# Kernel optimization log

Measured on AMD Instinct MI355X. Metric: run time of the kernel, lower is better.

Reference implementation:

```python
import jax, jax.numpy as jnp
import numpy as np

WIDTH = 256
HEAD = 16
SCALE = 2
G = WIDTH // HEAD          # 16 groups
NH = G * SCALE             # 32 kernelized heads
EPS = 1e-5
N_NODES = 20000
B_GRAPHS = 1024


def setup_inputs() -> dict:
    key = jax.random.key(0)
    ks = jax.random.split(key, 10)
    x = jax.random.normal(ks[0], (N_NODES, WIDTH), jnp.float32)
    x_res = jax.random.normal(ks[1], (B_GRAPHS, NH, HEAD, HEAD), jnp.float32)
    batch = jnp.sort(jax.random.randint(ks[2], (N_NODES,), 0, B_GRAPHS)).astype(jnp.int64)
    w_pre = jax.random.normal(ks[3], (WIDTH, WIDTH), jnp.float32) * 0.02
    b_pre = jnp.zeros((WIDTH,), jnp.float32)
    # grouped 1x1 convs: [groups, width_scale, head_out, head_in]
    wq = jax.random.normal(ks[4], (G, SCALE, HEAD, HEAD), jnp.float32) * 0.02
    wk = jax.random.normal(ks[5], (G, SCALE, HEAD, HEAD), jnp.float32) * 0.02
    wv = jax.random.normal(ks[6], (G, SCALE, HEAD, HEAD), jnp.float32) * 0.02
    w_post = jax.random.normal(ks[7], (WIDTH, WIDTH * SCALE), jnp.float32) * 0.02
    b_post = jnp.zeros((WIDTH,), jnp.float32)
    log_scale = jnp.full((WIDTH,), np.log(0.01), jnp.float32)
    return {"x": x, "x_res": x_res, "batch": batch, "batch_size": B_GRAPHS,
            "w_pre": w_pre, "b_pre": b_pre, "wq": wq, "wk": wk, "wv": wv,
            "w_post": w_post, "b_post": b_post, "log_scale": log_scale}


def reference(x, x_res, batch, batch_size, w_pre, b_pre, wq, wk, wv, w_post, b_post, log_scale):
    n = x.shape[0]
    # pre: 1x1 conv (= linear) + GroupNorm(affine=False); L=1 so normalize over
    # each group's width_head channels.
    y = x @ w_pre.T + b_pre                       # [N, width]
    yg = y.reshape(n, G, HEAD)                    # [N, G, Hd]
    mu = yg.mean(-1, keepdims=True)
    var = yg.var(-1, keepdims=True)               # biased, as in GroupNorm
    yn = (yg - mu) / jnp.sqrt(var + EPS)          # [N, G, Hd]

    inv_sqrt_h = 1.0 / np.sqrt(HEAD)
    # grouped convs -> kernelized q,k (exp) and v
    xq = jnp.exp(jnp.einsum('ngi,gsoi->ngso', yn, wq) * inv_sqrt_h).reshape(n, NH, HEAD)
    xk = jnp.exp(jnp.einsum('ngi,gsoi->ngso', yn, wk) * inv_sqrt_h).reshape(n, NH, HEAD)
    xv = jnp.einsum('ngi,gsoi->ngso', yn, wv).reshape(n, NH, HEAD)

    # outer product k (x) v then scatter-sum over graphs  [B, NH, Hd, Hd]
    kv = jnp.einsum('bnh,bnv->bnhv', xk, xv)
    kv_sum = jax.ops.segment_sum(kv, batch, num_segments=batch_size) + x_res
    x_res_out = kv_sum

    # per-graph key sum, gathered back to nodes
    k_sum = jax.ops.segment_sum(xk, batch, num_segments=batch_size)[batch]  # [N, NH, Hd]
    denom = jnp.einsum('bnh,bnh->bn', xq, k_sum)                            # [N, NH]
    qn = xq / denom[:, :, None]

    out = jnp.einsum('bnh,bnhv->bnv', qn, kv_sum[batch]).reshape(n, WIDTH * SCALE)
    out = jnp.exp(log_scale) * (out @ w_post.T + b_post)                    # [N, width]
    return (out, x_res_out)
```

## Files before the change

### kernel.cpp

```cpp
#include <hip/hip_runtime.h>
#include <stdint.h>

typedef unsigned int u32;
typedef unsigned short u16;
typedef __attribute__((ext_vector_type(8))) short v8s;
typedef __attribute__((ext_vector_type(4))) float v4f;

#define GN_EPS 1e-5f

__device__ __forceinline__ float bflo(u32 u){ return __uint_as_float(u << 16); }
__device__ __forceinline__ float bfhi(u32 u){ return __uint_as_float(u & 0xffff0000u); }
__device__ __forceinline__ float bf1(u16 u){ return __uint_as_float((u32)u << 16); }
__device__ __forceinline__ u16 f2bf(float f){
  u32 x = __float_as_uint(f);
  u32 r = (x + 0x7fffu + ((x >> 16) & 1u)) >> 16;
  return (u16)r;
}
__device__ __forceinline__ u32 pack2(float a, float b){
  return (u32)f2bf(a) | ((u32)f2bf(b) << 16);
}
__device__ __forceinline__ void unpack8(const uint4 u, float* f){
  f[0]=bflo(u.x); f[1]=bfhi(u.x); f[2]=bflo(u.y); f[3]=bfhi(u.y);
  f[4]=bflo(u.z); f[5]=bfhi(u.z); f[6]=bflo(u.w); f[7]=bfhi(u.w);
}
__device__ __forceinline__ uint4 loadpack8(const float* __restrict__ p){
  float4 a = *(const float4*)p, b = *(const float4*)(p + 4);
  return make_uint4(pack2(a.x,a.y),pack2(a.z,a.w),pack2(b.x,b.y),pack2(b.z,b.w));
}

__device__ __forceinline__ int getb(const int* __restrict__ b, int is64, int i){
  return b[is64 ? 2*i : i];
}

__global__ __launch_bounds__(256) void k_detect(
    const int* __restrict__ batch, int n, int* __restrict__ flags)
{
  int i = blockIdx.x*256 + threadIdx.x;
  int bad = 0;
  if (i < n - 1 && batch[i] > batch[i + 1]) bad = 1;
  if (__builtin_amdgcn_ballot_w64(bad) != 0 && (threadIdx.x & 63) == 0)
    atomicOr(&flags[0], 1);
}

__global__ __launch_bounds__(256) void k_bounds(
    const int* __restrict__ batch, const int* __restrict__ flags,
    int N, int B, int* __restrict__ bounds)
{
  int i = blockIdx.x*256 + threadIdx.x;
  if (i >= N) return;
  const int is64 = flags[0];
  int b = getb(batch, is64, i);
  int prev = (i == 0) ? -1 : getb(batch, is64, i - 1);
  for (int g = prev + 1; g <= b; g++) bounds[g] = i;
  if (i == N - 1)
    for (int g = b + 1; g <= B; g++) bounds[g] = N;
}

__global__ __launch_bounds__(256) void k_pre(
    const float* __restrict__ x, const float* __restrict__ wpre,
    const float* __restrict__ bpre, u16* __restrict__ y, int N, int nbm)
{
  __shared__ __align__(16) u16 As[128*40];
  __shared__ __align__(16) u16 Bs[64*40];
  const int t = threadIdx.x;
  const int bm = blockIdx.x % nbm;
  const int bn = blockIdx.x / nbm;
  const int m_base = bm*128, n_base = bn*64;
  const int w = t >> 6, lane = t & 63;
  const int wr = (w >> 1)*64, wc = (w & 1)*32;
  const int fr = lane & 15, fk = lane >> 4;
  const int arow = t >> 1, acol = (t & 1)*16;
  const int brow = t >> 2, bcol = (t & 3)*8;

  v4f acc[4][2];
#pragma unroll
  for (int i = 0; i < 4; i++)
#pragma unroll
    for (int j = 0; j < 2; j++) acc[i][j] = (v4f){0.f,0.f,0.f,0.f};

  for (int k0 = 0; k0 < 256; k0 += 32) {
    __syncthreads();
    {
      int gm = m_base + arow;
      uint4 a0 = make_uint4(0u,0u,0u,0u), a1 = make_uint4(0u,0u,0u,0u);
      if (gm < N) {
        a0 = loadpack8(x + (size_t)gm*256 + k0 + acol);
        a1 = loadpack8(x + (size_t)gm*256 + k0 + acol + 8);
      }
      *(uint4*)&As[arow*40 + acol]     = a0;
      *(uint4*)&As[arow*40 + acol + 8] = a1;
      uint4 bv = loadpack8(wpre + (size_t)(n_base + brow)*256 + k0 + bcol);
      *(uint4*)&Bs[brow*40 + bcol] = bv;
    }
    __syncthreads();
    v8s b0 = *(const v8s*)&Bs[(wc      + fr)*40 + fk*8];
    v8s b1 = *(const v8s*)&Bs[(wc + 16 + fr)*40 + fk*8];
#pragma unroll
    for (int mi = 0; mi < 4; mi++) {
      v8s a = *(const v8s*)&As[(wr + mi*16 + fr)*40 + fk*8];
      acc[mi][0] = __builtin_amdgcn_mfma_f32_16x16x32_bf16(a,b0,acc[mi][0],0,0,0);
      acc[mi][1] = __builtin_amdgcn_mfma_f32_16x16x32_bf16(a,b1,acc[mi][1],0,0,0);
    }
  }
#pragma unroll
  for (int nj = 0; nj < 2; nj++) {
    int col = n_base + wc + nj*16 + fr;
    float bpv = bpre[col];
#pragma unroll
    for (int mi = 0; mi < 4; mi++) {
#pragma unroll
      for (int r = 0; r < 4; r++) {
        int row = m_base + wr + mi*16 + fk*4 + r;
        if (row < N) y[(size_t)row*256 + col] = f2bf(acc[mi][nj][r] + bpv);
      }
    }
  }
}

__global__ __launch_bounds__(256) void k_gnqkv(
    const u16* __restrict__ y, const float* __restrict__ wq,
    const float* __restrict__ wk, const float* __restrict__ wv,
    u16* __restrict__ qo, u16* __restrict__ ko, u16* __restrict__ vo, int N)
{
  __shared__ __align__(16) float wL[3*512];
  const int t = threadIdx.x;
  const int g = blockIdx.x & 15;
  const int c = blockIdx.x >> 4;
  {
    const float* srcs[3] = {wq, wk, wv};
#pragma unroll
    for (int tz = 0; tz < 3; tz++) {
      wL[tz*512 + t]       = srcs[tz][g*512 + t];
      wL[tz*512 + t + 256] = srcs[tz][g*512 + t + 256];
    }
  }
  __syncthreads();
  const int node = c*256 + t;
  if (node >= N) return;

  const u16* yp = y + (size_t)node*256 + g*16;
  uint4 Y0 = *(const uint4*)yp;
  uint4 Y1 = *(const uint4*)(yp + 8);
  float a[16]; unpack8(Y0, a); unpack8(Y1, a + 8);
  float mu = 0.f;
#pragma unroll
  for (int i = 0; i < 16; i++) mu += a[i];
  mu *= 0.0625f;
  float s2 = 0.f;
#pragma unroll
  for (int i = 0; i < 16; i++) { float d = a[i]-mu; s2 = fmaf(d,d,s2); }
  float inv = rsqrtf(s2*0.0625f + GN_EPS);
  float yn[16];
#pragma unroll
  for (int i = 0; i < 16; i++) yn[i] = (a[i]-mu)*inv;

  u16* outs[3] = {qo, ko, vo};
#pragma unroll
  for (int tz = 0; tz < 3; tz++) {
#pragma unroll
    for (int s = 0; s < 2; s++) {
      u32 p[8];
#pragma unroll
      for (int o = 0; o < 16; o++) {
        const float* row = &wL[tz*512 + (s*16 + o)*16];
        float4 W0 = *(const float4*)row;
        float4 W1 = *(const float4*)(row + 4);
        float4 W2 = *(const float4*)(row + 8);
        float4 W3 = *(const float4*)(row + 12);
        float w[16] = {W0.x,W0.y,W0.z,W0.w,W1.x,W1.y,W1.z,W1.w,
                       W2.x,W2.y,W2.z,W2.w,W3.x,W3.y,W3.z,W3.w};
        float d = 0.f;
#pragma unroll
        for (int i = 0; i < 16; i++) d = fmaf(yn[i], w[i], d);
        if (tz < 2) d = __expf(d*0.25f);
        if (o & 1) p[o>>1] |= (u32)f2bf(d) << 16;
        else       p[o>>1]  = (u32)f2bf(d);
      }
      u16* dst = outs[tz] + (size_t)node*512 + g*32 + s*16;
      *(uint4*)dst       = make_uint4(p[0],p[1],p[2],p[3]);
      *(uint4*)(dst + 8) = make_uint4(p[4],p[5],p[6],p[7]);
    }
  }
}

__global__ __launch_bounds__(512) void k_segatt(
    const u16* __restrict__ xk, const u16* __restrict__ xv,
    const u16* __restrict__ xq, const float* __restrict__ xres,
    const int* __restrict__ bounds,
    float* __restrict__ out1, u16* __restrict__ att, int N)
{
  __shared__ __align__(16) u16 kvs[32*280];
  __shared__ float kss[32*17];
  const int b = blockIdx.x, t = threadIdx.x;
  const int lo = bounds[b], hi = bounds[b+1];
  const int nh = t >> 4, d = t & 15;

  float kv[16];
#pragma unroll
  for (int v = 0; v < 16; v++) kv[v] = 0.f;
  float ks = 0.f;

  const size_t koff = (size_t)nh*16 + d;
  const size_t voff = (size_t)nh*16;
  int node = lo;
  for (; node + 1 < hi; node += 2) {
    u16  ka  = xk[(size_t)node*512 + koff];
    uint4 Va0 = *(const uint4*)(xv + (size_t)node*512 + voff);
    uint4 Va1 = *(const uint4*)(xv + (size_t)node*512 + voff + 8);
    u16  kb  = xk[(size_t)(node+1)*512 + koff];
    uint4 Vb0 = *(const uint4*)(xv + (size_t)(node+1)*512 + voff);
    uint4 Vb1 = *(const uint4*)(xv + (size_t)(node+1)*512 + voff + 8);
    float k0 = bf1(ka), k1 = bf1(kb);
    float va[16], vb[16];
    unpack8(Va0, va); unpack8(Va1, va + 8);
    unpack8(Vb0, vb); unpack8(Vb1, vb + 8);
    ks += k0 + k1;
#pragma unroll
    for (int v = 0; v < 16; v++) {
      kv[v] = fmaf(k0, va[v], kv[v]);
      kv[v] = fmaf(k1, vb[v], kv[v]);
    }
  }
  if (node < hi) {
    u16  ka  = xk[(size_t)node*512 + koff];
    uint4 V0 = *(const uint4*)(xv + (size_t)node*512 + voff);
    uint4 V1 = *(const uint4*)(xv + (size_t)node*512 + voff + 8);
    float k0 = bf1(ka);
    float vf[16]; unpack8(V0, vf); unpack8(V1, vf + 8);
    ks += k0;
#pragma unroll
    for (int v = 0; v < 16; v++) kv[v] = fmaf(k0, vf[v], kv[v]);
  }

  kss[nh*17 + d] = ks;

  {
    size_t idx = ((size_t)(b*32 + nh)*16 + d)*16;
    const float* xp = xres + idx;
    float4 X0 = *(const float4*)xp;
    float4 X1 = *(const float4*)(xp + 4);
    float4 X2 = *(const float4*)(xp + 8);
    float4 X3 = *(const float4*)(xp + 12);
    float xf[16] = {X0.x,X0.y,X0.z,X0.w,X1.x,X1.y,X1.z,X1.w,
                    X2.x,X2.y,X2.z,X2.w,X3.x,X3.y,X3.z,X3.w};
    float o[16];
#pragma unroll
    for (int j = 0; j < 16; j++) o[j] = kv[j] + xf[j];
    float* op = out1 + idx;
    *(float4*)op        = make_float4(o[0],o[1],o[2],o[3]);
    *(float4*)(op + 4)  = make_float4(o[4],o[5],o[6],o[7]);
    *(float4*)(op + 8)  = make_float4(o[8],o[9],o[10],o[11]);
    *(float4*)(op + 12) = make_float4(o[12],o[13],o[14],o[15]);
    u16* lp = &kvs[nh*280 + d*16];
    *(uint4*)lp       = make_uint4(pack2(o[0],o[1]),  pack2(o[2],o[3]),
                                   pack2(o[4],o[5]),  pack2(o[6],o[7]));
    *(uint4*)(lp + 8) = make_uint4(pack2(o[8],o[9]),  pack2(o[10],o[11]),
                                   pack2(o[12],o[13]),pack2(o[14],o[15]));
  }
  __syncthreads();

  const int nh2 = t & 31, ns = t >> 5;
  for (int n0 = lo; n0 < hi; n0 += 16) {
    int nodei = n0 + ns;
    if (nodei >= hi) continue;
    const u16* qp = xq + (size_t)nodei*512 + nh2*16;
    uint4 Q0 = *(const uint4*)qp;
    uint4 Q1 = *(const uint4*)(qp + 8);
    float q[16]; unpack8(Q0, q); unpack8(Q1, q + 8);
    const float* ksp = &kss[nh2*17];
    float denom = 0.f;
#pragma unroll
    for (int i = 0; i < 16; i++) denom = fmaf(q[i], ksp[i], denom);
    float inv = 1.0f / fmaxf(denom, 1e-20f);
    float a[16];
#pragma unroll
    for (int v = 0; v < 16; v++) a[v] = 0.f;
    const u16* kvp = &kvs[nh2*280];
#pragma unroll
    for (int h = 0; h < 16; h++) {
      float qh = q[h] * inv;
      uint4 W0 = *(const uint4*)(kvp + h*16);
      uint4 W1 = *(const uint4*)(kvp + h*16 + 8);
      float w[16]; unpack8(W0, w); unpack8(W1, w + 8);
#pragma unroll
      for (int v = 0; v < 16; v++) a[v] = fmaf(qh, w[v], a[v]);
    }
    u32 p[8];
#pragma unroll
    for (int j = 0; j < 8; j++) p[j] = pack2(a[2*j], a[2*j+1]);
    u16* dst = att + (size_t)nodei*512 + nh2*16;
    *(uint4*)dst       = make_uint4(p[0],p[1],p[2],p[3]);
    *(uint4*)(dst + 8) = make_uint4(p[4],p[5],p[6],p[7]);
  }
}

__global__ __launch_bounds__(256) void k_post(
    const u16* __restrict__ att, const float* __restrict__ wpost,
    const float* __restrict__ bpost, const float* __restrict__ ls,
    float* __restrict__ out0, int N, int nbm)
{
  __shared__ __align__(16) u16 As[128*40];
  __shared__ __align__(16) u16 Bs[64*40];
  const int t = threadIdx.x;
  const int bm = blockIdx.x % nbm;
  const int bn = blockIdx.x / nbm;
  const int m_base = bm*128, n_base = bn*64;
  const int w = t >> 6, lane = t & 63;
  const int wr = (w >> 1)*64, wc = (w & 1)*32;
  const int fr = lane & 15, fk = lane >> 4;
  const int arow = t >> 1, acol = (t & 1)*16;
  const int brow = t >> 2, bcol = (t & 3)*8;

  v4f acc[4][2];
#pragma unroll
  for (int i = 0; i < 4; i++)
#pragma unroll
    for (int j = 0; j < 2; j++) acc[i][j] = (v4f){0.f,0.f,0.f,0.f};

  for (int k0 = 0; k0 < 512; k0 += 32) {
    __syncthreads();
    {
      int gm = m_base + arow;
      uint4 a0 = make_uint4(0u,0u,0u,0u), a1 = make_uint4(0u,0u,0u,0u);
      if (gm < N) {
        a0 = *(const uint4*)(att + (size_t)gm*512 + k0 + acol);
        a1 = *(const uint4*)(att + (size_t)gm*512 + k0 + acol + 8);
      }
      *(uint4*)&As[arow*40 + acol]     = a0;
      *(uint4*)&As[arow*40 + acol + 8] = a1;
      uint4 bv = loadpack8(wpost + (size_t)(n_base + brow)*512 + k0 + bcol);
      *(uint4*)&Bs[brow*40 + bcol] = bv;
    }
    __syncthreads();
    v8s b0 = *(const v8s*)&Bs[(wc      + fr)*40 + fk*8];
    v8s b1 = *(const v8s*)&Bs[(wc + 16 + fr)*40 + fk*8];
#pragma unroll
    for (int mi = 0; mi < 4; mi++) {
      v8s a = *(const v8s*)&As[(wr + mi*16 + fr)*40 + fk*8];
      acc[mi][0] = __builtin_amdgcn_mfma_f32_16x16x32_bf16(a,b0,acc[mi][0],0,0,0);
      acc[mi][1] = __builtin_amdgcn_mfma_f32_16x16x32_bf16(a,b1,acc[mi][1],0,0,0);
    }
  }
#pragma unroll
  for (int nj = 0; nj < 2; nj++) {
    int col = n_base + wc + nj*16 + fr;
    float bpv = bpost[col];
    float e   = __expf(ls[col]);
#pragma unroll
    for (int mi = 0; mi < 4; mi++) {
#pragma unroll
      for (int r = 0; r < 4; r++) {
        int row = m_base + wr + mi*16 + fk*4 + r;
        if (row < N) out0[(size_t)row*256 + col] = e*(acc[mi][nj][r] + bpv);
      }
    }
  }
}

extern "C" void kernel_launch(void* const* d_in, const int* in_sizes, int n_in,
                              void* d_out, int out_size, void* d_ws, size_t ws_size,
                              hipStream_t stream)
{
  const float* x     = (const float*)d_in[0];
  const float* xres  = (const float*)d_in[1];
  const int*   batch = (const int*)d_in[2];
  const float* wpre  = (const float*)d_in[4];
  const float* bpre  = (const float*)d_in[5];
  const float* wq    = (const float*)d_in[6];
  const float* wk    = (const float*)d_in[7];
  const float* wv    = (const float*)d_in[8];
  const float* wpost = (const float*)d_in[9];
  const float* bpost = (const float*)d_in[10];
  const float* ls    = (const float*)d_in[11];

  const int N = in_sizes[0] / 256;
  const int B = in_sizes[1] / 8192;
  const int nbm = (N + 127) / 128;
  const int nchunk = (N + 255) / 256;

  char* ws = (char*)d_ws;
  size_t off = 0;
  int*   flags  = (int*)(ws + off); off += 256;
  int*   bounds = (int*)(ws + off); off += ((size_t)B + 64) * 4;
  u16*   y      = (u16*)(ws + off);  off += (size_t)N * 512;
  u16*   att    = (u16*)(ws + off);  off += (size_t)N * 1024;
  u16*   q      = (u16*)(ws + off);  off += (size_t)N * 1024;
  u16*   kten   = (u16*)(ws + off);  off += (size_t)N * 1024;
  u16*   vten   = (u16*)(ws + off);  off += (size_t)N * 1024;

  float* out0 = (float*)d_out;
  float* out1 = out0 + (size_t)N * 256;

  hipMemsetAsync(flags, 0, 4, stream);
  k_detect<<<nchunk,         256, 0, stream>>>(batch, N, flags);
  k_bounds<<<nchunk,         256, 0, stream>>>(batch, flags, N, B, bounds);
  k_pre   <<<nbm * 4,        256, 0, stream>>>(x, wpre, bpre, y, N, nbm);
  k_gnqkv <<<nchunk * 16,    256, 0, stream>>>(y, wq, wk, wv, q, kten, vten, N);
  k_segatt<<<B,              512, 0, stream>>>(kten, vten, q, xres, bounds,
                                               out1, att, N);
  k_post  <<<nbm * 4,        256, 0, stream>>>(att, wpost, bpost, ls, out0, N, nbm);
}
```

Measured before the change: 130.8 us.

## Fuse pre-linear GEMM with GroupNorm and grouped QKV projection

Merges the pre-projection GEMM and the GroupNorm plus q/k/v grouped-conv kernel into one kernel. GroupNorm statistics are computed from the MFMA accumulators with 16-lane shuffle reductions, the normalized values go to shared memory, and each block then computes q/k/v for its 4 groups using weights staged in reused LDS. This removes the bf16 y intermediate round trip through global memory and one launch. In exchange it adds LDS pressure, a single-pass variance formula, and only 128 nodes x 4 groups of projection work per block.

```diff
diff --git a/kernel.cpp b/kernel.cpp
--- a/kernel.cpp
+++ b/kernel.cpp
@@ -26,6 +26,30 @@
 __device__ __forceinline__ uint4 loadpack8(const float* __restrict__ p){
   float4 a = *(const float4*)p, b = *(const float4*)(p + 4);
   return make_uint4(pack2(a.x,a.y),pack2(a.z,a.w),pack2(b.x,b.y),pack2(b.z,b.w));
+}
+__device__ __forceinline__ float dot16(const float* __restrict__ yn,
+                                       const float* __restrict__ row){
+  float4 W0 = *(const float4*)row;
+  float4 W1 = *(const float4*)(row + 4);
+  float4 W2 = *(const float4*)(row + 8);
+  float4 W3 = *(const float4*)(row + 12);
+  float d = 0.f;
+  d = fmaf(yn[0],W0.x,d); d = fmaf(yn[1],W0.y,d);
+  d = fmaf(yn[2],W0.z,d); d = fmaf(yn[3],W0.w,d);
+  d = fmaf(yn[4],W1.x,d); d = fmaf(yn[5],W1.y,d);
+  d = fmaf(yn[6],W1.z,d); d = fmaf(yn[7],W1.w,d);
+  d = fmaf(yn[8],W2.x,d); d = fmaf(yn[9],W2.y,d);
+  d = fmaf(yn[10],W2.z,d); d = fmaf(yn[11],W2.w,d);
+  d = fmaf(yn[12],W3.x,d); d = fmaf(yn[13],W3.y,d);
+  d = fmaf(yn[14],W3.z,d); d = fmaf(yn[15],W3.w,d);
+  return d;
+}
+__device__ __forceinline__ float rsum16(float v){
+  v += __shfl_xor(v, 1);
+  v += __shfl_xor(v, 2);
+  v += __shfl_xor(v, 4);
+  v += __shfl_xor(v, 8);
+  return v;
 }
 
 __device__ __forceinline__ int getb(const int* __restrict__ b, int is64, int i){
@@ -56,12 +80,20 @@
     for (int g = b + 1; g <= B; g++) bounds[g] = N;
 }
 
-__global__ __launch_bounds__(256) void k_pre(
+__global__ __launch_bounds__(256) void k_prefused(
     const float* __restrict__ x, const float* __restrict__ wpre,
-    const float* __restrict__ bpre, u16* __restrict__ y, int N, int nbm)
-{
-  __shared__ __align__(16) u16 As[128*40];
-  __shared__ __align__(16) u16 Bs[64*40];
+    const float* __restrict__ bpre,
+    const float* __restrict__ wq, const float* __restrict__ wk,
+    const float* __restrict__ wv,
+    u16* __restrict__ qo, u16* __restrict__ ko, u16* __restrict__ vo,
+    int N, int nbm)
+{
+  __shared__ __align__(16) char SMEM[25600];
+  __shared__ __align__(16) u16 ynL[128*72];
+  u16* As = (u16*)SMEM;
+  u16* Bs = (u16*)(SMEM + 128*40*2);
+  float* wL = (float*)SMEM;
+
   const int t = threadIdx.x;
   const int bm = blockIdx.x % nbm;
   const int bn = blockIdx.x / nbm;
@@ -102,83 +134,68 @@
       acc[mi][1] = __builtin_amdgcn_mfma_f32_16x16x32_bf16(a,b1,acc[mi][1],0,0,0);
     }
   }
+
 #pragma unroll
   for (int nj = 0; nj < 2; nj++) {
     int col = n_base + wc + nj*16 + fr;
     float bpv = bpre[col];
+    int gloc = (w & 1)*2 + nj;
 #pragma unroll
     for (int mi = 0; mi < 4; mi++) {
 #pragma unroll
       for (int r = 0; r < 4; r++) {
-        int row = m_base + wr + mi*16 + fk*4 + r;
-        if (row < N) y[(size_t)row*256 + col] = f2bf(acc[mi][nj][r] + bpv);
-      }
-    }
-  }
-}
-
-__global__ __launch_bounds__(256) void k_gnqkv(
-    const u16* __restrict__ y, const float* __restrict__ wq,
-    const float* __restrict__ wk, const float* __restrict__ wv,
-    u16* __restrict__ qo, u16* __restrict__ ko, u16* __restrict__ vo, int N)
-{
-  __shared__ __align__(16) float wL[3*512];
-  const int t = threadIdx.x;
-  const int g = blockIdx.x & 15;
-  const int c = blockIdx.x >> 4;
+        float yv = acc[mi][nj][r] + bpv;
+        float s1 = rsum16(yv);
+        float s2 = rsum16(yv*yv);
+        float mu = s1 * 0.0625f;
+        float var = fmaxf(s2*0.0625f - mu*mu, 0.f);
+        float ynv = (yv - mu) * rsqrtf(var + GN_EPS);
+        int row = wr + mi*16 + fk*4 + r;
+        ynL[row*72 + gloc*16 + fr] = f2bf(ynv);
+      }
+    }
+  }
+  __syncthreads();
+
   {
     const float* srcs[3] = {wq, wk, wv};
 #pragma unroll
     for (int tz = 0; tz < 3; tz++) {
-      wL[tz*512 + t]       = srcs[tz][g*512 + t];
-      wL[tz*512 + t + 256] = srcs[tz][g*512 + t + 256];
+      for (int i = t; i < 2048; i += 256) {
+        int gi = i >> 9, rem = i & 511;
+        wL[tz*2080 + gi*520 + rem] = srcs[tz][((size_t)(bn*4 + gi))*512 + rem];
+      }
     }
   }
   __syncthreads();
-  const int node = c*256 + t;
-  if (node >= N) return;
-
-  const u16* yp = y + (size_t)node*256 + g*16;
-  uint4 Y0 = *(const uint4*)yp;
-  uint4 Y1 = *(const uint4*)(yp + 8);
-  float a[16]; unpack8(Y0, a); unpack8(Y1, a + 8);
-  float mu = 0.f;
-#pragma unroll
-  for (int i = 0; i < 16; i++) mu += a[i];
-  mu *= 0.0625f;
-  float s2 = 0.f;
-#pragma unroll
-  for (int i = 0; i < 16; i++) { float d = a[i]-mu; s2 = fmaf(d,d,s2); }
-  float inv = rsqrtf(s2*0.0625f + GN_EPS);
-  float yn[16];
-#pragma unroll
-  for (int i = 0; i < 16; i++) yn[i] = (a[i]-mu)*inv;
 
   u16* outs[3] = {qo, ko, vo};
 #pragma unroll
-  for (int tz = 0; tz < 3; tz++) {
-#pragma unroll
-    for (int s = 0; s < 2; s++) {
-      u32 p[8];
-#pragma unroll
-      for (int o = 0; o < 16; o++) {
-        const float* row = &wL[tz*512 + (s*16 + o)*16];
-        float4 W0 = *(const float4*)row;
-        float4 W1 = *(const float4*)(row + 4);
-        float4 W2 = *(const float4*)(row + 8);
-        float4 W3 = *(const float4*)(row + 12);
-        float w[16] = {W0.x,W0.y,W0.z,W0.w,W1.x,W1.y,W1.z,W1.w,
-                       W2.x,W2.y,W2.z,W2.w,W3.x,W3.y,W3.z,W3.w};
-        float d = 0.f;
-#pragma unroll
-        for (int i = 0; i < 16; i++) d = fmaf(yn[i], w[i], d);
-        if (tz < 2) d = __expf(d*0.25f);
-        if (o & 1) p[o>>1] |= (u32)f2bf(d) << 16;
-        else       p[o>>1]  = (u32)f2bf(d);
-      }
-      u16* dst = outs[tz] + (size_t)node*512 + g*32 + s*16;
-      *(uint4*)dst       = make_uint4(p[0],p[1],p[2],p[3]);
-      *(uint4*)(dst + 8) = make_uint4(p[4],p[5],p[6],p[7]);
+  for (int p = 0; p < 2; p++) {
+    int idx = p*256 + t;
+    int nloc = idx >> 2, gl = idx & 3;
+    int node = m_base + nloc;
+    if (node >= N) continue;
+    uint4 Y0 = *(const uint4*)&ynL[nloc*72 + gl*16];
+    uint4 Y1 = *(const uint4*)&ynL[nloc*72 + gl*16 + 8];
+    float yn[16]; unpack8(Y0, yn); unpack8(Y1, yn + 8);
+    int g = bn*4 + gl;
+#pragma unroll
+    for (int tz = 0; tz < 3; tz++) {
+#pragma unroll
+      for (int s = 0; s < 2; s++) {
+        u32 pk[8];
+#pragma unroll
+        for (int o = 0; o < 16; o++) {
+          float d = dot16(yn, &wL[tz*2080 + gl*520 + (s*16 + o)*16]);
+          if (tz < 2) d = __expf(d*0.25f);
+          if (o & 1) pk[o>>1] |= (u32)f2bf(d) << 16;
+          else       pk[o>>1]  = (u32)f2bf(d);
+        }
+        u16* dst = outs[tz] + (size_t)node*512 + g*32 + s*16;
+        *(uint4*)dst       = make_uint4(pk[0],pk[1],pk[2],pk[3]);
+        *(uint4*)(dst + 8) = make_uint4(pk[4],pk[5],pk[6],pk[7]);
+      }
     }
   }
 }
@@ -281,9 +298,9 @@
       float qh = q[h] * inv;
       uint4 W0 = *(const uint4*)(kvp + h*16);
       uint4 W1 = *(const uint4*)(kvp + h*16 + 8);
-      float w[16]; unpack8(W0, w); unpack8(W1, w + 8);
-#pragma unroll
-      for (int v = 0; v < 16; v++) a[v] = fmaf(qh, w[v], a[v]);
+      float wv2[16]; unpack8(W0, wv2); unpack8(W1, wv2 + 8);
+#pragma unroll
+      for (int v = 0; v < 16; v++) a[v] = fmaf(qh, wv2[v], a[v]);
     }
     u32 p[8];
 #pragma unroll
@@ -382,7 +399,6 @@
   size_t off = 0;
   int*   flags  = (int*)(ws + off); off += 256;
   int*   bounds = (int*)(ws + off); off += ((size_t)B + 64) * 4;
-  u16*   y      = (u16*)(ws + off);  off += (size_t)N * 512;
   u16*   att    = (u16*)(ws + off);  off += (size_t)N * 1024;
   u16*   q      = (u16*)(ws + off);  off += (size_t)N * 1024;
   u16*   kten   = (u16*)(ws + off);  off += (size_t)N * 1024;
@@ -392,11 +408,11 @@
   float* out1 = out0 + (size_t)N * 256;
 
   hipMemsetAsync(flags, 0, 4, stream);
-  k_detect<<<nchunk,         256, 0, stream>>>(batch, N, flags);
-  k_bounds<<<nchunk,         256, 0, stream>>>(batch, flags, N, B, bounds);
-  k_pre   <<<nbm * 4,        256, 0, stream>>>(x, wpre, bpre, y, N, nbm);
-  k_gnqkv <<<nchunk * 16,    256, 0, stream>>>(y, wq, wk, wv, q, kten, vten, N);
-  k_segatt<<<B,              512, 0, stream>>>(kten, vten, q, xres, bounds,
-                                               out1, att, N);
-  k_post  <<<nbm * 4,        256, 0, stream>>>(att, wpost, bpost, ls, out0, N, nbm);
-}
+  k_detect  <<<nchunk,        256, 0, stream>>>(batch, N, flags);
+  k_bounds  <<<nchunk,        256, 0, stream>>>(batch, flags, N, B, bounds);
+  k_prefused<<<nbm * 4,       256, 0, stream>>>(x, wpre, bpre, wq, wk, wv,
+                                                q, kten, vten, N, nbm);
+  k_segatt  <<<B,             512, 0, stream>>>(kten, vten, q, xres, bounds,
+                                                out1, att, N);
+  k_post    <<<nbm * 4,       256, 0, stream>>>(att, wpost, bpost, ls, out0, N, nbm);
+}
```

Measured after the change: 128.2 us. Within noise of the previous version (-2.0%).
